# Kernel optimization log

Measured on AMD Instinct MI355X. Metric: run time of the kernel, lower is better.

The kernel has to match this reference:

```python
import jax, jax.numpy as jnp
import numpy as np

N_NODES = 100000


def gcn_layer(x, edge_index, W, b, num_nodes):
    # GCNConv (PyG): h = x @ W; add self-loops; symmetric deg^-1/2 norm; scatter-add; + bias
    h = x @ W  # [N, out]
    loops = jnp.arange(num_nodes, dtype=edge_index.dtype)
    src = jnp.concatenate([edge_index[0], loops])
    dst = jnp.concatenate([edge_index[1], loops])
    deg = jax.ops.segment_sum(jnp.ones(src.shape[0], dtype=h.dtype), dst,
                              num_segments=num_nodes)  # includes self-loop, so deg >= 1
    dis = jax.lax.rsqrt(deg)  # deg^-1/2
    norm = dis[src] * dis[dst]  # [E+N]
    msg = h[src] * norm[:, None]  # gather + scale
    out = jax.ops.segment_sum(msg, dst, num_segments=num_nodes)  # scatter-add
    return out + b


def setup_inputs() -> dict:
    key = jax.random.key(0)
    k1, k2, k3, k4 = jax.random.split(key, 4)
    num_feature, hidden, num_label = 512, 16, 40
    n_edges = 3200000
    x = jax.random.normal(k1, (N_NODES, num_feature), dtype=jnp.float32)
    edge_index = jax.random.randint(k2, (2, n_edges), 0, N_NODES, dtype=jnp.int64)
    # Glorot-style init for weights
    W1 = jax.random.normal(k3, (num_feature, hidden), dtype=jnp.float32) / np.sqrt(num_feature)
    b1 = jnp.zeros((hidden,), dtype=jnp.float32)
    W2 = jax.random.normal(k4, (hidden, num_label), dtype=jnp.float32) / np.sqrt(hidden)
    b2 = jnp.zeros((num_label,), dtype=jnp.float32)
    return {"x": x, "edge_index": edge_index, "W1": W1, "b1": b1, "W2": W2, "b2": b2}


def reference(x, edge_index, W1, b1, W2, b2):
    h = gcn_layer(x, edge_index, W1, b1, N_NODES)
    h = jax.nn.relu(h)
    # dropout is identity in eval mode
    h = gcn_layer(h, edge_index, W2, b2, N_NODES)
    return jax.nn.log_softmax(h, axis=1)
```

## Files before the change

kernel.cpp:

```cpp
#include <hip/hip_runtime.h>
#include <math.h>

#define N_NODES 100000
#define N_EDGES 3200000
#define F_IN    512
#define H1      16
#define H2      40

#define NB      391
#define BSH     8
#define BMASK   255
#define B1      512
#define EPB     6250
#define CAP     9216

__global__ void detect_idx_kernel(const int* __restrict__ ei, int* __restrict__ flag,
                                  int* __restrict__ cnt)
{
    for (int i = threadIdx.x; i < 512; i += 64) cnt[i] = 0;
    if (threadIdx.x == 0) {
        int all_zero = 1;
        for (int i = 0; i < 64; ++i)
            if (ei[2 * i + 1] != 0) { all_zero = 0; break; }
        *flag = all_zero;
    }
}

__device__ __forceinline__ int edge_src(const void* ei, int e, int is64)
{
    return is64 ? (int)((const long long*)ei)[e] : ((const int*)ei)[e];
}
__device__ __forceinline__ int edge_dst(const void* ei, int e, int is64)
{
    return is64 ? (int)((const long long*)ei)[N_EDGES + e]
                : ((const int*)ei)[N_EDGES + e];
}

__global__ __launch_bounds__(256) void scatter_atomic_kernel(
    const void* __restrict__ ei, const int* __restrict__ flag,
    int* __restrict__ cnt, int* __restrict__ packed)
{
    __shared__ int h[NB];
    __shared__ int cur[NB];
    for (int i = threadIdx.x; i < NB; i += 256) h[i] = 0;
    __syncthreads();
    const int is64 = *flag;
    const int e0 = blockIdx.x * EPB;
    for (int i = threadIdx.x; i < EPB; i += 256) {
        int e = e0 + i;
        if (e < N_EDGES) atomicAdd(&h[edge_dst(ei, e, is64) >> BSH], 1);
    }
    __syncthreads();
    for (int i = threadIdx.x; i < NB; i += 256) {
        int base = (h[i] > 0) ? atomicAdd(&cnt[i], h[i]) : 0;
        cur[i] = i * CAP + base;
    }
    __syncthreads();
    for (int i = threadIdx.x; i < EPB; i += 256) {
        int e = e0 + i;
        if (e >= N_EDGES) break;
        const int s = edge_src(ei, e, is64);
        const int d = edge_dst(ei, e, is64);
        const int pos = atomicAdd(&cur[d >> BSH], 1);
        packed[pos] = (s << BSH) | (d & BMASK);
    }
}

__global__ __launch_bounds__(512) void bucket_csr_kernel(
    const int* __restrict__ packed, const int* __restrict__ cnt,
    int* __restrict__ deg, int* __restrict__ row_beg, int* __restrict__ csr)
{
    __shared__ int hist[256];
    __shared__ int off[256];
    __shared__ int sbase;
    const int b   = blockIdx.x;
    const int tid = threadIdx.x;

    if (tid < 64) {
        int s = 0;
        for (int i = tid; i < b; i += 64) s += cnt[i];
        #pragma unroll
        for (int o = 32; o > 0; o >>= 1) s += __shfl_xor(s, o, 64);
        if (tid == 0) sbase = s;
    }
    if (tid < 256) hist[tid] = 0;
    __syncthreads();

    const int base_in = b * CAP;
    const int m       = cnt[b];
    for (int i = tid; i < m; i += 512)
        atomicAdd(&hist[packed[base_in + i] & BMASK], 1);
    __syncthreads();

    int v = 0;
    if (tid < 256) { v = hist[tid]; off[tid] = v; }
    __syncthreads();
    for (int o = 1; o < 256; o <<= 1) {
        int t2 = 0;
        if (tid < 256 && tid >= o) t2 = off[tid - o];
        __syncthreads();
        if (tid < 256) off[tid] += t2;
        __syncthreads();
    }
    if (tid < 256) {
        const int excl = sbase + off[tid] - v;
        const int g = (b << BSH) + tid;
        if (g < N_NODES) { deg[g] = v; row_beg[g] = excl; }
        off[tid] = excl;
    }
    __syncthreads();
    for (int i = tid; i < m; i += 512) {
        const int p = packed[base_in + i];
        const int pos = atomicAdd(&off[p & BMASK], 1);
        csr[pos] = p >> BSH;
    }
}

__global__ __launch_bounds__(256) void gemm1_kernel(
    const float* __restrict__ x, const float* __restrict__ W1,
    const int* __restrict__ deg, float* __restrict__ hs1,
    float* __restrict__ dis, int n)
{
    const int r = blockIdx.x * 256 + threadIdx.x;
    if (r >= n) return;

    const float4* xr = (const float4*)(x + (size_t)r * F_IN);
    float acc[H1];
    #pragma unroll
    for (int j = 0; j < H1; ++j) acc[j] = 0.f;

    #pragma unroll 2
    for (int k4 = 0; k4 < F_IN / 4; ++k4) {
        const float4 xv = xr[k4];
        const float* wk = W1 + k4 * 4 * H1;
        #pragma unroll
        for (int j = 0; j < H1; ++j)
            acc[j] += xv.x * wk[j] + xv.y * wk[H1 + j]
                    + xv.z * wk[2 * H1 + j] + xv.w * wk[3 * H1 + j];
    }

    const float dv = rsqrtf((float)deg[r] + 1.0f);
    dis[r] = dv;
    float4* o = (float4*)(hs1 + (size_t)r * H1);
    #pragma unroll
    for (int q = 0; q < 4; ++q) {
        float4 v;
        v.x = acc[4 * q + 0] * dv;
        v.y = acc[4 * q + 1] * dv;
        v.z = acc[4 * q + 2] * dv;
        v.w = acc[4 * q + 3] * dv;
        o[q] = v;
    }
}

__global__ __launch_bounds__(256) void pull1_kernel(
    const int* __restrict__ row_beg, const int* __restrict__ deg,
    const int* __restrict__ csr, const float* __restrict__ rows,
    const float* __restrict__ dis, const float* __restrict__ b1,
    float* __restrict__ out, int n)
{
    int t = blockIdx.x * 256 + threadIdx.x;
    int g = t >> 2;
    int q = t & 3;
    if (g >= n) return;
    const int beg = row_beg[g];
    const int end = beg + deg[g];
    float4 a0 = make_float4(0.f, 0.f, 0.f, 0.f);
    float4 a1 = make_float4(0.f, 0.f, 0.f, 0.f);
    int i = beg;
    for (; i + 3 < end; i += 4) {
        const int s0 = csr[i], s1 = csr[i + 1], s2 = csr[i + 2], s3 = csr[i + 3];
        float4 v0 = ((const float4*)(rows + (size_t)s0 * H1))[q];
        float4 v1 = ((const float4*)(rows + (size_t)s1 * H1))[q];
        float4 v2 = ((const float4*)(rows + (size_t)s2 * H1))[q];
        float4 v3 = ((const float4*)(rows + (size_t)s3 * H1))[q];
        a0.x += v0.x + v2.x; a0.y += v0.y + v2.y; a0.z += v0.z + v2.z; a0.w += v0.w + v2.w;
        a1.x += v1.x + v3.x; a1.y += v1.y + v3.y; a1.z += v1.z + v3.z; a1.w += v1.w + v3.w;
    }
    for (; i < end; ++i) {
        float4 v = ((const float4*)(rows + (size_t)csr[i] * H1))[q];
        a0.x += v.x; a0.y += v.y; a0.z += v.z; a0.w += v.w;
    }
    a0.x += a1.x; a0.y += a1.y; a0.z += a1.z; a0.w += a1.w;

    const float dv = dis[g];
    float4 h = ((const float4*)(rows + (size_t)g * H1))[q];
    float4 bq = ((const float4*)b1)[q];
    a0.x = dv * fmaxf(dv * (a0.x + h.x) + bq.x, 0.f);
    a0.y = dv * fmaxf(dv * (a0.y + h.y) + bq.y, 0.f);
    a0.z = dv * fmaxf(dv * (a0.z + h.z) + bq.z, 0.f);
    a0.w = dv * fmaxf(dv * (a0.w + h.w) + bq.w, 0.f);
    ((float4*)(out + (size_t)g * H1))[q] = a0;
}

__global__ __launch_bounds__(256) void pull2_epi_kernel(
    const int* __restrict__ row_beg, const int* __restrict__ deg,
    const int* __restrict__ csr, const float* __restrict__ c,
    const float* __restrict__ W2, const float* __restrict__ b2,
    const float* __restrict__ dis, float* __restrict__ out, int n)
{
    __shared__ float w[H1 * H2];
    __shared__ float bb[H2];
    for (int i = threadIdx.x; i < H1 * H2; i += 256) w[i] = W2[i];
    if (threadIdx.x < H2) bb[threadIdx.x] = b2[threadIdx.x];
    __syncthreads();

    int t = blockIdx.x * 256 + threadIdx.x;
    int g = t >> 2;
    int q = t & 3;
    if (g >= n) return;
    const int beg = row_beg[g];
    const int end = beg + deg[g];
    float4 a0 = make_float4(0.f, 0.f, 0.f, 0.f);
    float4 a1 = make_float4(0.f, 0.f, 0.f, 0.f);
    int i = beg;
    for (; i + 3 < end; i += 4) {
        const int s0 = csr[i], s1 = csr[i + 1], s2 = csr[i + 2], s3 = csr[i + 3];
        float4 v0 = ((const float4*)(c + (size_t)s0 * H1))[q];
        float4 v1 = ((const float4*)(c + (size_t)s1 * H1))[q];
        float4 v2 = ((const float4*)(c + (size_t)s2 * H1))[q];
        float4 v3 = ((const float4*)(c + (size_t)s3 * H1))[q];
        a0.x += v0.x + v2.x; a0.y += v0.y + v2.y; a0.z += v0.z + v2.z; a0.w += v0.w + v2.w;
        a1.x += v1.x + v3.x; a1.y += v1.y + v3.y; a1.z += v1.z + v3.z; a1.w += v1.w + v3.w;
    }
    for (; i < end; ++i) {
        float4 v = ((const float4*)(c + (size_t)csr[i] * H1))[q];
        a0.x += v.x; a0.y += v.y; a0.z += v.z; a0.w += v.w;
    }
    float4 sv = ((const float4*)(c + (size_t)g * H1))[q];
    float4 acc;
    acc.x = a0.x + a1.x + sv.x;
    acc.y = a0.y + a1.y + sv.y;
    acc.z = a0.z + a1.z + sv.z;
    acc.w = a0.w + a1.w + sv.w;

    float tt[16];
    tt[4 * q + 0] = acc.x; tt[4 * q + 1] = acc.y;
    tt[4 * q + 2] = acc.z; tt[4 * q + 3] = acc.w;
    #pragma unroll
    for (int p = 1; p < 4; ++p) {
        const int qq = q ^ p;
        tt[4 * qq + 0] = __shfl_xor(acc.x, p, 64);
        tt[4 * qq + 1] = __shfl_xor(acc.y, p, 64);
        tt[4 * qq + 2] = __shfl_xor(acc.z, p, 64);
        tt[4 * qq + 3] = __shfl_xor(acc.w, p, 64);
    }

    const float dv = dis[g];
    float val[10];
    float m = -INFINITY;
    #pragma unroll
    for (int u = 0; u < 10; ++u) {
        const int j = q * 10 + u;
        float s = 0.f;
        #pragma unroll
        for (int k = 0; k < H1; ++k) s += tt[k] * w[k * H2 + j];
        val[u] = dv * s + bb[j];
        m = fmaxf(m, val[u]);
    }
    m = fmaxf(m, __shfl_xor(m, 1, 64));
    m = fmaxf(m, __shfl_xor(m, 2, 64));
    float ex = 0.f;
    #pragma unroll
    for (int u = 0; u < 10; ++u) ex += __expf(val[u] - m);
    ex += __shfl_xor(ex, 1, 64);
    ex += __shfl_xor(ex, 2, 64);
    const float lse = m + logf(ex);

    float2* o = (float2*)(out + (size_t)g * H2 + q * 10);
    #pragma unroll
    for (int u = 0; u < 5; ++u) {
        float2 v;
        v.x = val[2 * u]     - lse;
        v.y = val[2 * u + 1] - lse;
        o[u] = v;
    }
}

extern "C" void kernel_launch(void* const* d_in, const int* in_sizes, int n_in,
                              void* d_out, int out_size, void* d_ws, size_t ws_size,
                              hipStream_t stream)
{
    const float* x   = (const float*)d_in[0];
    const void*  ei  = d_in[1];
    const float* W1  = (const float*)d_in[2];
    const float* b1  = (const float*)d_in[3];
    const float* W2  = (const float*)d_in[4];
    const float* b2  = (const float*)d_in[5];
    float*       out = (float*)d_out;

    int*   base    = (int*)d_ws;
    int*   flag    = base;
    int*   deg     = base + 16;
    int*   row_beg = deg + N_NODES;
    int*   cnt     = row_beg + N_NODES;
    float* dis     = (float*)(cnt + 512);
    int*   csr     = (int*)(dis + N_NODES);
    int*   packed  = csr + N_EDGES;
    float* hs1     = (float*)packed;
    float* c       = hs1 + (size_t)N_NODES * H1;

    detect_idx_kernel<<<1, 64, 0, stream>>>((const int*)ei, flag, cnt);

    scatter_atomic_kernel<<<B1, 256, 0, stream>>>(ei, flag, cnt, packed);
    bucket_csr_kernel<<<NB, 512, 0, stream>>>(packed, cnt, deg, row_beg, csr);

    gemm1_kernel<<<(N_NODES + 255) / 256, 256, 0, stream>>>(x, W1, deg, hs1, dis, N_NODES);

    const int PB = (N_NODES * 4 + 255) / 256;
    pull1_kernel<<<PB, 256, 0, stream>>>(row_beg, deg, csr, hs1, dis, b1, c, N_NODES);
    pull2_epi_kernel<<<PB, 256, 0, stream>>>(row_beg, deg, csr, c, W2, b2, dis, out, N_NODES);
}
```

Before: 261.8 us.

## Replace CSR build and pull aggregation with bucket-local shared-memory atomic accumulation

Drops the per-bucket prefix scan and CSR construction, keeping only a degree histogram. Both aggregation layers now work per destination bucket of 256 nodes, gathering source rows from the packed bucket list and accumulating them with LDS float atomics into a rotated per-node shared tile. This removes the CSR scatter pass and the row_beg/csr reads, in exchange for many shared-memory atomics. Only 391 blocks run, which limits parallelism, and the float sums become order-nondeterministic.

```diff
diff --git a/kernel.cpp b/kernel.cpp
--- a/kernel.cpp
+++ b/kernel.cpp
@@ -61,58 +61,26 @@
         if (e >= N_EDGES) break;
         const int s = edge_src(ei, e, is64);
         const int d = edge_dst(ei, e, is64);
-        const int pos = atomicAdd(&cur[d >> BSH], 1);
-        packed[pos] = (s << BSH) | (d & BMASK);
-    }
-}
-
-__global__ __launch_bounds__(512) void bucket_csr_kernel(
+        int pos = atomicAdd(&cur[d >> BSH], 1);
+        if (pos < NB * CAP) packed[pos] = (s << BSH) | (d & BMASK);
+    }
+}
+
+__global__ __launch_bounds__(512) void deg_hist_kernel(
     const int* __restrict__ packed, const int* __restrict__ cnt,
-    int* __restrict__ deg, int* __restrict__ row_beg, int* __restrict__ csr)
+    int* __restrict__ deg)
 {
     __shared__ int hist[256];
-    __shared__ int off[256];
-    __shared__ int sbase;
-    const int b   = blockIdx.x;
-    const int tid = threadIdx.x;
-
-    if (tid < 64) {
-        int s = 0;
-        for (int i = tid; i < b; i += 64) s += cnt[i];
-        #pragma unroll
-        for (int o = 32; o > 0; o >>= 1) s += __shfl_xor(s, o, 64);
-        if (tid == 0) sbase = s;
-    }
+    const int b = blockIdx.x, tid = threadIdx.x;
     if (tid < 256) hist[tid] = 0;
     __syncthreads();
-
-    const int base_in = b * CAP;
-    const int m       = cnt[b];
+    const int m = cnt[b], base = b * CAP;
     for (int i = tid; i < m; i += 512)
-        atomicAdd(&hist[packed[base_in + i] & BMASK], 1);
-    __syncthreads();
-
-    int v = 0;
-    if (tid < 256) { v = hist[tid]; off[tid] = v; }
-    __syncthreads();
-    for (int o = 1; o < 256; o <<= 1) {
-        int t2 = 0;
-        if (tid < 256 && tid >= o) t2 = off[tid - o];
-        __syncthreads();
-        if (tid < 256) off[tid] += t2;
-        __syncthreads();
-    }
+        atomicAdd(&hist[packed[base + i] & BMASK], 1);
+    __syncthreads();
     if (tid < 256) {
-        const int excl = sbase + off[tid] - v;
         const int g = (b << BSH) + tid;
-        if (g < N_NODES) { deg[g] = v; row_beg[g] = excl; }
-        off[tid] = excl;
-    }
-    __syncthreads();
-    for (int i = tid; i < m; i += 512) {
-        const int p = packed[base_in + i];
-        const int pos = atomicAdd(&off[p & BMASK], 1);
-        csr[pos] = p >> BSH;
+        if (g < N_NODES) deg[g] = hist[tid];
     }
 }
 
@@ -153,127 +121,130 @@
     }
 }
 
-__global__ __launch_bounds__(256) void pull1_kernel(
-    const int* __restrict__ row_beg, const int* __restrict__ deg,
-    const int* __restrict__ csr, const float* __restrict__ rows,
-    const float* __restrict__ dis, const float* __restrict__ b1,
-    float* __restrict__ out, int n)
-{
-    int t = blockIdx.x * 256 + threadIdx.x;
-    int g = t >> 2;
-    int q = t & 3;
-    if (g >= n) return;
-    const int beg = row_beg[g];
-    const int end = beg + deg[g];
-    float4 a0 = make_float4(0.f, 0.f, 0.f, 0.f);
-    float4 a1 = make_float4(0.f, 0.f, 0.f, 0.f);
-    int i = beg;
-    for (; i + 3 < end; i += 4) {
-        const int s0 = csr[i], s1 = csr[i + 1], s2 = csr[i + 2], s3 = csr[i + 3];
-        float4 v0 = ((const float4*)(rows + (size_t)s0 * H1))[q];
-        float4 v1 = ((const float4*)(rows + (size_t)s1 * H1))[q];
-        float4 v2 = ((const float4*)(rows + (size_t)s2 * H1))[q];
-        float4 v3 = ((const float4*)(rows + (size_t)s3 * H1))[q];
-        a0.x += v0.x + v2.x; a0.y += v0.y + v2.y; a0.z += v0.z + v2.z; a0.w += v0.w + v2.w;
-        a1.x += v1.x + v3.x; a1.y += v1.y + v3.y; a1.z += v1.z + v3.z; a1.w += v1.w + v3.w;
-    }
-    for (; i < end; ++i) {
-        float4 v = ((const float4*)(rows + (size_t)csr[i] * H1))[q];
-        a0.x += v.x; a0.y += v.y; a0.z += v.z; a0.w += v.w;
-    }
-    a0.x += a1.x; a0.y += a1.y; a0.z += a1.z; a0.w += a1.w;
-
+__global__ __launch_bounds__(512) void agg1_kernel(
+    const int* __restrict__ packed, const int* __restrict__ cnt,
+    const float* __restrict__ hs1, const float* __restrict__ dis,
+    const float* __restrict__ b1, float* __restrict__ c)
+{
+    __shared__ float accL[256 * H1];
+    __shared__ float bb[H1];
+    const int b = blockIdx.x, tid = threadIdx.x;
+    #pragma unroll
+    for (int u = 0; u < 8; ++u) accL[tid * 8 + u] = 0.f;
+    if (tid < H1) bb[tid] = b1[tid];
+    __syncthreads();
+
+    const int m = cnt[b], base = b * CAP;
+    const int q = tid & 3;
+    for (int i = tid >> 2; i < m; i += 128) {
+        const int p   = packed[base + i];
+        const int s   = p >> BSH;
+        const int nd  = p & BMASK;
+        const float4 v = *(const float4*)(hs1 + (size_t)s * H1 + q * 4);
+        atomicAdd(&accL[nd * H1 + ((4 * q + 0 + nd) & 15)], v.x);
+        atomicAdd(&accL[nd * H1 + ((4 * q + 1 + nd) & 15)], v.y);
+        atomicAdd(&accL[nd * H1 + ((4 * q + 2 + nd) & 15)], v.z);
+        atomicAdd(&accL[nd * H1 + ((4 * q + 3 + nd) & 15)], v.w);
+    }
+    __syncthreads();
+
+    const int nd = tid >> 1;
+    const int e0 = (tid & 1) * 8;
+    const int g  = (b << BSH) + nd;
+    if (g >= N_NODES) return;
     const float dv = dis[g];
-    float4 h = ((const float4*)(rows + (size_t)g * H1))[q];
-    float4 bq = ((const float4*)b1)[q];
-    a0.x = dv * fmaxf(dv * (a0.x + h.x) + bq.x, 0.f);
-    a0.y = dv * fmaxf(dv * (a0.y + h.y) + bq.y, 0.f);
-    a0.z = dv * fmaxf(dv * (a0.z + h.z) + bq.z, 0.f);
-    a0.w = dv * fmaxf(dv * (a0.w + h.w) + bq.w, 0.f);
-    ((float4*)(out + (size_t)g * H1))[q] = a0;
-}
-
-__global__ __launch_bounds__(256) void pull2_epi_kernel(
-    const int* __restrict__ row_beg, const int* __restrict__ deg,
-    const int* __restrict__ csr, const float* __restrict__ c,
+    float o[8];
+    #pragma unroll
+    for (int u = 0; u < 8; ++u) {
+        const int e = e0 + u;
+        const float t = accL[nd * H1 + ((e + nd) & 15)]
+                      + hs1[(size_t)g * H1 + e];
+        o[u] = dv * fmaxf(dv * t + bb[e], 0.f);
+    }
+    float4* op = (float4*)(c + (size_t)g * H1 + e0);
+    op[0] = make_float4(o[0], o[1], o[2], o[3]);
+    op[1] = make_float4(o[4], o[5], o[6], o[7]);
+}
+
+__global__ __launch_bounds__(512) void agg2_kernel(
+    const int* __restrict__ packed, const int* __restrict__ cnt,
+    const float* __restrict__ c, const float* __restrict__ dis,
     const float* __restrict__ W2, const float* __restrict__ b2,
-    const float* __restrict__ dis, float* __restrict__ out, int n)
-{
+    float* __restrict__ out)
+{
+    __shared__ float accL[256 * H1];
     __shared__ float w[H1 * H2];
     __shared__ float bb[H2];
-    for (int i = threadIdx.x; i < H1 * H2; i += 256) w[i] = W2[i];
-    if (threadIdx.x < H2) bb[threadIdx.x] = b2[threadIdx.x];
-    __syncthreads();
-
-    int t = blockIdx.x * 256 + threadIdx.x;
-    int g = t >> 2;
-    int q = t & 3;
-    if (g >= n) return;
-    const int beg = row_beg[g];
-    const int end = beg + deg[g];
-    float4 a0 = make_float4(0.f, 0.f, 0.f, 0.f);
-    float4 a1 = make_float4(0.f, 0.f, 0.f, 0.f);
-    int i = beg;
-    for (; i + 3 < end; i += 4) {
-        const int s0 = csr[i], s1 = csr[i + 1], s2 = csr[i + 2], s3 = csr[i + 3];
-        float4 v0 = ((const float4*)(c + (size_t)s0 * H1))[q];
-        float4 v1 = ((const float4*)(c + (size_t)s1 * H1))[q];
-        float4 v2 = ((const float4*)(c + (size_t)s2 * H1))[q];
-        float4 v3 = ((const float4*)(c + (size_t)s3 * H1))[q];
-        a0.x += v0.x + v2.x; a0.y += v0.y + v2.y; a0.z += v0.z + v2.z; a0.w += v0.w + v2.w;
-        a1.x += v1.x + v3.x; a1.y += v1.y + v3.y; a1.z += v1.z + v3.z; a1.w += v1.w + v3.w;
-    }
-    for (; i < end; ++i) {
-        float4 v = ((const float4*)(c + (size_t)csr[i] * H1))[q];
-        a0.x += v.x; a0.y += v.y; a0.z += v.z; a0.w += v.w;
-    }
-    float4 sv = ((const float4*)(c + (size_t)g * H1))[q];
-    float4 acc;
-    acc.x = a0.x + a1.x + sv.x;
-    acc.y = a0.y + a1.y + sv.y;
-    acc.z = a0.z + a1.z + sv.z;
-    acc.w = a0.w + a1.w + sv.w;
-
-    float tt[16];
-    tt[4 * q + 0] = acc.x; tt[4 * q + 1] = acc.y;
-    tt[4 * q + 2] = acc.z; tt[4 * q + 3] = acc.w;
-    #pragma unroll
-    for (int p = 1; p < 4; ++p) {
-        const int qq = q ^ p;
-        tt[4 * qq + 0] = __shfl_xor(acc.x, p, 64);
-        tt[4 * qq + 1] = __shfl_xor(acc.y, p, 64);
-        tt[4 * qq + 2] = __shfl_xor(acc.z, p, 64);
-        tt[4 * qq + 3] = __shfl_xor(acc.w, p, 64);
-    }
-
-    const float dv = dis[g];
-    float val[10];
-    float m = -INFINITY;
-    #pragma unroll
-    for (int u = 0; u < 10; ++u) {
-        const int j = q * 10 + u;
-        float s = 0.f;
-        #pragma unroll
-        for (int k = 0; k < H1; ++k) s += tt[k] * w[k * H2 + j];
-        val[u] = dv * s + bb[j];
-        m = fmaxf(m, val[u]);
-    }
-    m = fmaxf(m, __shfl_xor(m, 1, 64));
-    m = fmaxf(m, __shfl_xor(m, 2, 64));
-    float ex = 0.f;
-    #pragma unroll
-    for (int u = 0; u < 10; ++u) ex += __expf(val[u] - m);
-    ex += __shfl_xor(ex, 1, 64);
-    ex += __shfl_xor(ex, 2, 64);
-    const float lse = m + logf(ex);
-
-    float2* o = (float2*)(out + (size_t)g * H2 + q * 10);
-    #pragma unroll
-    for (int u = 0; u < 5; ++u) {
-        float2 v;
-        v.x = val[2 * u]     - lse;
-        v.y = val[2 * u + 1] - lse;
-        o[u] = v;
+    const int b = blockIdx.x, tid = threadIdx.x;
+    #pragma unroll
+    for (int u = 0; u < 8; ++u) accL[tid * 8 + u] = 0.f;
+    for (int i = tid; i < H1 * H2; i += 512) w[i] = W2[i];
+    if (tid < H2) bb[tid] = b2[tid];
+    __syncthreads();
+
+    const int m = cnt[b], base = b * CAP;
+    const int q = tid & 3;
+    for (int i = tid >> 2; i < m; i += 128) {
+        const int p   = packed[base + i];
+        const int s   = p >> BSH;
+        const int nd  = p & BMASK;
+        const float4 v = *(const float4*)(c + (size_t)s * H1 + q * 4);
+        atomicAdd(&accL[nd * H1 + ((4 * q + 0 + nd) & 15)], v.x);
+        atomicAdd(&accL[nd * H1 + ((4 * q + 1 + nd) & 15)], v.y);
+        atomicAdd(&accL[nd * H1 + ((4 * q + 2 + nd) & 15)], v.z);
+        atomicAdd(&accL[nd * H1 + ((4 * q + 3 + nd) & 15)], v.w);
+    }
+    __syncthreads();
+
+    {
+        const int nd = tid >> 1;
+        const int e0 = (tid & 1) * 8;
+        const int g  = (b << BSH) + nd;
+        if (g < N_NODES) {
+            #pragma unroll
+            for (int u = 0; u < 8; ++u) {
+                const int e = e0 + u;
+                accL[nd * H1 + ((e + nd) & 15)] += c[(size_t)g * H1 + e];
+            }
+        }
+    }
+    __syncthreads();
+
+    for (int gl = tid >> 2; gl < 256; gl += 128) {
+        const int g = (b << BSH) + gl;
+        if (g >= N_NODES) continue;
+        float tt[H1];
+        #pragma unroll
+        for (int k = 0; k < H1; ++k)
+            tt[k] = accL[gl * H1 + ((k + gl) & 15)];
+        const float dv = dis[g];
+        float val[10];
+        float mx = -INFINITY;
+        #pragma unroll
+        for (int u = 0; u < 10; ++u) {
+            const int j = q * 10 + u;
+            float s = 0.f;
+            #pragma unroll
+            for (int k = 0; k < H1; ++k) s += tt[k] * w[k * H2 + j];
+            val[u] = dv * s + bb[j];
+            mx = fmaxf(mx, val[u]);
+        }
+        mx = fmaxf(mx, __shfl_xor(mx, 1, 64));
+        mx = fmaxf(mx, __shfl_xor(mx, 2, 64));
+        float ex = 0.f;
+        #pragma unroll
+        for (int u = 0; u < 10; ++u) ex += __expf(val[u] - mx);
+        ex += __shfl_xor(ex, 1, 64);
+        ex += __shfl_xor(ex, 2, 64);
+        const float lse = mx + logf(ex);
+        float2* o = (float2*)(out + (size_t)g * H2 + q * 10);
+        #pragma unroll
+        for (int u = 0; u < 5; ++u) {
+            float2 v;
+            v.x = val[2 * u]     - lse;
+            v.y = val[2 * u + 1] - lse;
+            o[u] = v;
+        }
     }
 }
 
@@ -291,23 +262,20 @@
 
     int*   base    = (int*)d_ws;
     int*   flag    = base;
-    int*   deg     = base + 16;
-    int*   row_beg = deg + N_NODES;
-    int*   cnt     = row_beg + N_NODES;
-    float* dis     = (float*)(cnt + 512);
-    int*   csr     = (int*)(dis + N_NODES);
-    int*   packed  = csr + N_EDGES;
-    float* hs1     = (float*)packed;
+    int*   cnt     = base + 16;
+    int*   deg     = cnt + 512;
+    float* dis     = (float*)(deg + N_NODES);
+    float* hs1     = dis + N_NODES;
     float* c       = hs1 + (size_t)N_NODES * H1;
+    int*   packed  = (int*)(c + (size_t)N_NODES * H1);
 
     detect_idx_kernel<<<1, 64, 0, stream>>>((const int*)ei, flag, cnt);
 
     scatter_atomic_kernel<<<B1, 256, 0, stream>>>(ei, flag, cnt, packed);
-    bucket_csr_kernel<<<NB, 512, 0, stream>>>(packed, cnt, deg, row_beg, csr);
+    deg_hist_kernel<<<NB, 512, 0, stream>>>(packed, cnt, deg);
 
     gemm1_kernel<<<(N_NODES + 255) / 256, 256, 0, stream>>>(x, W1, deg, hs1, dis, N_NODES);
 
-    const int PB = (N_NODES * 4 + 255) / 256;
-    pull1_kernel<<<PB, 256, 0, stream>>>(row_beg, deg, csr, hs1, dis, b1, c, N_NODES);
-    pull2_epi_kernel<<<PB, 256, 0, stream>>>(row_beg, deg, csr, c, W2, b2, dis, out, N_NODES);
-}
+    agg1_kernel<<<NB, 512, 0, stream>>>(packed, cnt, hs1, dis, b1, c);
+    agg2_kernel<<<NB, 512, 0, stream>>>(packed, cnt, c, dis, W2, b2, out);
+}
```

New measurement: 812.3 us. 3.1x slower.

## Stage x tiles into LDS with async global_load_lds double buffering in gemm1

Applied to the files above, without the earlier changes.

Rewrites the first-layer GEMM so each 128-thread block copies W1 into shared memory and streams 32-column tiles of x into a double-buffered LDS area using direct global-to-LDS loads with an XOR swizzle. Each thread then reads its row from LDS and accumulates with FMAs. Previously every thread read its own 2KB row with strided float4 loads, which coalesce poorly across lanes. The new version adds manual waitcnt and barrier handling, and the 32KB W1 copy plus the tile buffers use a large amount of LDS, which may limit occupancy.

```diff
diff --git a/kernel.cpp b/kernel.cpp
--- a/kernel.cpp
+++ b/kernel.cpp
@@ -13,6 +13,10 @@
 #define B1      512
 #define EPB     6250
 #define CAP     9216
+
+#define GR      128
+#define GKT     32
+#define GNT     (F_IN / GKT)
 
 __global__ void detect_idx_kernel(const int* __restrict__ ei, int* __restrict__ flag,
                                   int* __restrict__ cnt)
@@ -116,40 +120,88 @@
     }
 }
 
-__global__ __launch_bounds__(256) void gemm1_kernel(
+__global__ __launch_bounds__(128) void gemm1_kernel(
     const float* __restrict__ x, const float* __restrict__ W1,
     const int* __restrict__ deg, float* __restrict__ hs1,
     float* __restrict__ dis, int n)
 {
-    const int r = blockIdx.x * 256 + threadIdx.x;
-    if (r >= n) return;
-
-    const float4* xr = (const float4*)(x + (size_t)r * F_IN);
+    __shared__ float wsh[F_IN * H1];
+    __shared__ __attribute__((aligned(16))) float xt[2][GR * GKT];
+
+    const int tid = threadIdx.x;
+    const int wv  = tid >> 6;
+    const int ln  = tid & 63;
+    const int r0  = blockIdx.x * GR;
+
+    for (int i = tid; i < F_IN * H1 / 4; i += 128)
+        ((float4*)wsh)[i] = ((const float4*)W1)[i];
+
+    const int lrow  = ln >> 3;
+    const int lslot = ln & 7;
+    const int gslot = lslot ^ lrow;
+
+    auto issue = [&](int kt, int buf) {
+        #pragma unroll
+        for (int ii = 0; ii < 8; ++ii) {
+            const int row_l = wv * 64 + ii * 8 + lrow;
+            int row_g = r0 + row_l;
+            if (row_g > n - 1) row_g = n - 1;
+            const float* g = x + (size_t)row_g * F_IN + kt * GKT + gslot * 4;
+            float* l = &xt[buf][(wv * 64 + ii * 8) * GKT];
+            __builtin_amdgcn_global_load_lds(
+                (const __attribute__((address_space(1))) void*)g,
+                (__attribute__((address_space(3))) void*)l,
+                16, 0, 0);
+        }
+    };
+
     float acc[H1];
     #pragma unroll
     for (int j = 0; j < H1; ++j) acc[j] = 0.f;
 
-    #pragma unroll 2
-    for (int k4 = 0; k4 < F_IN / 4; ++k4) {
-        const float4 xv = xr[k4];
-        const float* wk = W1 + k4 * 4 * H1;
-        #pragma unroll
-        for (int j = 0; j < H1; ++j)
-            acc[j] += xv.x * wk[j] + xv.y * wk[H1 + j]
-                    + xv.z * wk[2 * H1 + j] + xv.w * wk[3 * H1 + j];
-    }
-
-    const float dv = rsqrtf((float)deg[r] + 1.0f);
-    dis[r] = dv;
-    float4* o = (float4*)(hs1 + (size_t)r * H1);
-    #pragma unroll
-    for (int q = 0; q < 4; ++q) {
-        float4 v;
-        v.x = acc[4 * q + 0] * dv;
-        v.y = acc[4 * q + 1] * dv;
-        v.z = acc[4 * q + 2] * dv;
-        v.w = acc[4 * q + 3] * dv;
-        o[q] = v;
+    __syncthreads();
+    issue(0, 0);
+
+    for (int kt = 0; kt < GNT; ++kt) {
+        const int buf = kt & 1;
+        if (kt + 1 < GNT) {
+            issue(kt + 1, buf ^ 1);
+            asm volatile("s_waitcnt vmcnt(8)" ::: "memory");
+        } else {
+            asm volatile("s_waitcnt vmcnt(0)" ::: "memory");
+        }
+        __builtin_amdgcn_s_barrier();
+        __builtin_amdgcn_sched_barrier(0);
+        #pragma unroll
+        for (int c = 0; c < 8; ++c) {
+            const float4 xv =
+                *(const float4*)&xt[buf][tid * GKT + ((c ^ (tid & 7)) << 2)];
+            const float* wk = wsh + (kt * GKT + c * 4) * H1;
+            #pragma unroll
+            for (int j = 0; j < H1; ++j) {
+                acc[j] = fmaf(xv.x, wk[j],          acc[j]);
+                acc[j] = fmaf(xv.y, wk[H1 + j],     acc[j]);
+                acc[j] = fmaf(xv.z, wk[2 * H1 + j], acc[j]);
+                acc[j] = fmaf(xv.w, wk[3 * H1 + j], acc[j]);
+            }
+        }
+        __builtin_amdgcn_s_barrier();
+    }
+
+    const int r = r0 + tid;
+    if (r < n) {
+        const float dv = rsqrtf((float)deg[r] + 1.0f);
+        dis[r] = dv;
+        float4* o = (float4*)(hs1 + (size_t)r * H1);
+        #pragma unroll
+        for (int q = 0; q < 4; ++q) {
+            float4 v;
+            v.x = acc[4 * q + 0] * dv;
+            v.y = acc[4 * q + 1] * dv;
+            v.z = acc[4 * q + 2] * dv;
+            v.w = acc[4 * q + 3] * dv;
+            o[q] = v;
+        }
     }
 }
 
@@ -305,7 +357,7 @@
     scatter_atomic_kernel<<<B1, 256, 0, stream>>>(ei, flag, cnt, packed);
     bucket_csr_kernel<<<NB, 512, 0, stream>>>(packed, cnt, deg, row_beg, csr);
 
-    gemm1_kernel<<<(N_NODES + 255) / 256, 256, 0, stream>>>(x, W1, deg, hs1, dis, N_NODES);
+    gemm1_kernel<<<(N_NODES + GR - 1) / GR, 128, 0, stream>>>(x, W1, deg, hs1, dis, N_NODES);
 
     const int PB = (N_NODES * 4 + 255) / 256;
     pull1_kernel<<<PB, 256, 0, stream>>>(row_beg, deg, csr, hs1, dis, b1, c, N_NODES);
```

Measured after the change: 304.6 us. 1.16x slower.
